# Performance work log

Measured on AMD Instinct MI355X. Metric: run time of the kernel, lower is better.

Reference implementation:

```python
import jax, jax.numpy as jnp
import numpy as np

L = 256
C = 20
B = 4096


def _pairwise_mask(L, C):
    # mask[l1, c1, l2, c2] = (l2 - l1 >= 1), independent of c1, c2
    ls = np.arange(L)
    m = (ls[None, :] - ls[:, None]) >= 1            # (L, L)
    mask = np.broadcast_to(m[:, None, :, None], (L, C, L, C))
    return jnp.asarray(mask[None], dtype=bool)       # (1, L, C, L, C)


def setup_inputs() -> dict:
    key = jax.random.key(0)
    k1, k2, k3, k4 = jax.random.split(key, 4)
    # one-hot sequences, flattened to (B, L*C) like the layer's input
    seq = jax.random.randint(k1, (B, L), 0, C)
    x_lc = jax.nn.one_hot(seq, C, dtype=jnp.float32).reshape(B, L * C)
    theta_0 = jax.random.normal(k2, (1,), dtype=jnp.float32)
    theta_lc = (jax.random.normal(k3, (1, L, C), dtype=jnp.float32)
                / np.sqrt(L).astype(np.float32))
    mask = _pairwise_mask(L, C)
    theta_lclc = (jax.random.normal(k4, (1, L, C, L, C), dtype=jnp.float32)
                  / np.float32(L)) * mask
    return {"x_lc": x_lc, "theta_0": theta_0, "theta_lc": theta_lc,
            "theta_lclc": theta_lclc, "mask": mask}


def reference(x_lc, theta_0, theta_lc, theta_lclc, mask):
    # x_lc: (B, L*C); reshape to (B, L, C)
    x = x_lc.reshape(-1, L, C)
    # additive term: sum over (l, c)
    phi = theta_0 + jnp.einsum('blc,lc->b', x, theta_lc[0])[:, None]  # (B, 1)
    # masked pairwise quadratic form: x^T (theta * mask) x, computed as a
    # GEMM instead of materializing the (B, L, C, L, C) broadcast tensor.
    Theta = (theta_lclc[0] * mask[0].astype(theta_lclc.dtype)).reshape(L * C, L * C)
    xf = x_lc  # (B, L*C)
    quad = jnp.sum((xf @ Theta) * xf, axis=1, keepdims=True)  # (B, 1)
    return phi + quad
```

## Files before the change

kernel.cpp:

```cpp
#include <hip/hip_runtime.h>

#define LPOS 256
#define CCH 20
#define BB 4096
#define LC 5120


__global__ __launch_bounds__(256) void k_prepare(
    const float* __restrict__ x_lc, const float* __restrict__ theta_0,
    const float* __restrict__ theta_lc, unsigned char* __restrict__ seqC,
    float* __restrict__ out)
{
    const int b = blockIdx.x;
    const int l = threadIdx.x;
    const float* xp = x_lc + (size_t)b * LC + (size_t)l * CCH;
    const float4* xp4 = reinterpret_cast<const float4*>(xp);
    float v[CCH];
#pragma unroll
    for (int q = 0; q < 5; ++q) {
        float4 t = xp4[q];
        v[q * 4 + 0] = t.x; v[q * 4 + 1] = t.y;
        v[q * 4 + 2] = t.z; v[q * 4 + 3] = t.w;
    }
    int s = 0; float best = v[0];
#pragma unroll
    for (int c = 1; c < CCH; ++c) { if (v[c] > best) { best = v[c]; s = c; } }

    seqC[(size_t)(l >> 4) * (BB * 16) + (size_t)b * 16 + (l & 15)] =
        (unsigned char)s;

    float lin = theta_lc[l * CCH + s];
#pragma unroll
    for (int off = 32; off > 0; off >>= 1) lin += __shfl_down(lin, off, 64);
    __shared__ float partial[4];
    const int wave = threadIdx.x >> 6;
    const int lane = threadIdx.x & 63;
    if (lane == 0) partial[wave] = lin;
    __syncthreads();
    if (threadIdx.x == 0)
        out[b] = theta_0[0] + partial[0] + partial[1] + partial[2] + partial[3];
}

#define QT 512
#define TBL 6400
#define NCHT 2160
#define NBLK 1024
#define NHEAVY 112

template <int MODE>
__global__ __launch_bounds__(QT, 8) void k_quad(
    const float* __restrict__ Theta,
    const uint4* __restrict__ seqC,
    float* __restrict__ part,
    float* __restrict__ out)
{
    __shared__ float Tl[TBL];

    const int blk = blockIdx.x;
    const int tid = threadIdx.x;
    const int wave = tid >> 6;
    const int lane = tid & 63;

    const int cnt   = (blk < NHEAVY) ? 3 : 2;
    const int start = (blk < NHEAVY) ? 3 * blk : 3 * NHEAVY + 2 * (blk - NHEAVY);

    int cl1[3], cm[3], cjl[3];
    {
        int T = start, l1 = 0;
        for (; l1 < 255; ++l1) {
            const int c = 16 - ((l1 + 1) >> 4);
            if (T < c) break;
            T -= c;
        }
        int m = ((l1 + 1) >> 4) + T;
#pragma unroll
        for (int d = 0; d < 3; ++d) {
            cl1[d] = l1; cm[d] = m;
            cjl[d] = (m == ((l1 + 1) >> 4)) ? ((l1 + 1) & 15) : 0;
            ++m;
            if (m == 16) { ++l1; m = (l1 + 1) >> 4; }
        }
    }

    auto stage = [&](int l1, int m) {
#pragma unroll
        for (int k = 0; k < 4; ++k) {
            const int seg = wave + 8 * k;
            if (seg < 25) {
                const int u = seg * 64 + lane;
                const int r = u / 5, cc = u - r * 5;
                const int j = r / CCH, s1 = r - j * CCH;
                const float* gp = Theta + (size_t)(l1 * CCH + s1) * LC
                                        + (m * 16 + j) * CCH + cc * 4;
                float* lp = Tl + seg * 256;
                __builtin_amdgcn_global_load_lds(
                    (const __attribute__((address_space(1))) void*)gp,
                    (__attribute__((address_space(3))) void*)lp, 16, 0, 0);
            }
        }
    };
    int basev[8];
    auto loadbase = [&](int l1) {
        const int mw = l1 >> 4;
        const int wsel = (l1 >> 2) & 3;
        const int sh = (l1 & 3) * 8;
#pragma unroll
        for (int i = 0; i < 8; ++i) {
            const uint4 u = seqC[(size_t)mw * BB + i * QT + tid];
            const unsigned w = (wsel == 0) ? u.x : (wsel == 1) ? u.y
                             : (wsel == 2) ? u.z : u.w;
            basev[i] = (int)((w >> sh) & 0xFFu) * CCH;
        }
    };

    float acc[8];
#pragma unroll
    for (int i = 0; i < 8; ++i) acc[i] = 0.f;

    auto gather = [&](int d) {
        const int jl = cjl[d];
        const size_t mrow = (size_t)cm[d] * BB;
        if (jl == 0) {
#pragma unroll
            for (int i = 0; i < 8; ++i) {
                const uint4 u = seqC[mrow + i * QT + tid];
#pragma unroll
                for (int j = 0; j < 16; ++j) {
                    const unsigned w = (j < 4) ? u.x : (j < 8) ? u.y
                                     : (j < 12) ? u.z : u.w;
                    const int s2 = (w >> ((j & 3) * 8)) & 0xFF;
                    acc[i] += Tl[j * 400 + basev[i] + s2];
                }
            }
        } else {
#pragma unroll
            for (int i = 0; i < 8; ++i) {
                const uint4 u = seqC[mrow + i * QT + tid];
#pragma unroll
                for (int j = 0; j < 16; ++j) {
                    const unsigned w = (j < 4) ? u.x : (j < 8) ? u.y
                                     : (j < 12) ? u.z : u.w;
                    const int s2 = (w >> ((j & 3) * 8)) & 0xFF;
                    const float v = Tl[j * 400 + basev[i] + s2];
                    acc[i] += (j >= jl) ? v : 0.f;
                }
            }
        }
    };

    int curl1 = cl1[0];
    stage(cl1[0], cm[0]);
    loadbase(cl1[0]);
    __syncthreads();
    gather(0);
    for (int d = 1; d < cnt; ++d) {
        __syncthreads();
        stage(cl1[d], cm[d]);
        if (cl1[d] != curl1) { loadbase(cl1[d]); curl1 = cl1[d]; }
        __syncthreads();
        gather(d);
    }

    if (MODE == 0) {
        float* row = part + (size_t)blk * BB;
#pragma unroll
        for (int i = 0; i < 8; ++i) row[i * QT + tid] = acc[i];
    } else {
#pragma unroll
        for (int i = 0; i < 8; ++i) atomicAdd(&out[i * QT + tid], acc[i]);
    }
}

__global__ __launch_bounds__(256) void k_reduce(
    const float4* __restrict__ part4,
    float* __restrict__ out)
{
    const int b4 = blockIdx.x * 256 + threadIdx.x;
    const int r0 = blockIdx.y * 16;
    float4 a = make_float4(0.f, 0.f, 0.f, 0.f);
    for (int r = r0; r < r0 + 16; ++r) {
        const float4 p = part4[(size_t)r * 1024 + b4];
        a.x += p.x; a.y += p.y; a.z += p.z; a.w += p.w;
    }
    atomicAdd(&out[b4 * 4 + 0], a.x);
    atomicAdd(&out[b4 * 4 + 1], a.y);
    atomicAdd(&out[b4 * 4 + 2], a.z);
    atomicAdd(&out[b4 * 4 + 3], a.w);
}

extern "C" void kernel_launch(void* const* d_in, const int* in_sizes, int n_in,
                              void* d_out, int out_size, void* d_ws, size_t ws_size,
                              hipStream_t stream) {
    const float* x_lc       = (const float*)d_in[0];
    const float* theta_0    = (const float*)d_in[1];
    const float* theta_lc   = (const float*)d_in[2];
    const float* theta_lclc = (const float*)d_in[3];
    float* out = (float*)d_out;

    unsigned char* seqC = (unsigned char*)d_ws;
    float* part = (float*)((char*)d_ws + (1 << 20));
    const size_t need = (1 << 20) + (size_t)NBLK * BB * 4;

    k_prepare<<<dim3(BB), dim3(256), 0, stream>>>(x_lc, theta_0, theta_lc, seqC, out);
    if (ws_size >= need) {
        k_quad<0><<<dim3(NBLK), dim3(QT), 0, stream>>>(
            theta_lclc, (const uint4*)seqC, part, out);
        k_reduce<<<dim3(4, 64), dim3(256), 0, stream>>>(
            (const float4*)part, out);
    } else {
        k_quad<1><<<dim3(NBLK), dim3(QT), 0, stream>>>(
            theta_lclc, (const uint4*)seqC, part, out);
    }
}
```

Measured before the change: 70.59 us.

## Replace static chunk assignment with atomic work-stealing queue in quad kernel

Static per-block assignment of 2 or 3 chunks is replaced by a global atomic counter, so blocks dynamically grab chunk indices. A precomputed chunkinfo table, filled by extra blocks in the prepare kernel, holds the (l1, m, jl) decoding for each chunk. The goal is better load balance across CUs than the fixed 3/2 split. In exchange it adds a memset launch, one atomic per chunk, and an extra barrier per iteration. It also loses the structured reuse of basev between consecutive chunks, since a block's chunks are no longer contiguous.

```diff
diff --git a/kernel.cpp b/kernel.cpp
--- a/kernel.cpp
+++ b/kernel.cpp
@@ -5,12 +5,34 @@
 #define BB 4096
 #define LC 5120
 
+#define QT 512
+#define TBL 6400
+#define NCHT 2160
+#define NBLK 1024
+#define NPREPX 9
+
 
 __global__ __launch_bounds__(256) void k_prepare(
     const float* __restrict__ x_lc, const float* __restrict__ theta_0,
     const float* __restrict__ theta_lc, unsigned char* __restrict__ seqC,
-    float* __restrict__ out)
+    unsigned* __restrict__ chunkinfo, float* __restrict__ out)
 {
+    if (blockIdx.x >= BB) {
+        const int idx = (blockIdx.x - BB) * 256 + threadIdx.x;
+        if (idx < NCHT) {
+            int T = idx, l1 = 0;
+            for (; l1 < 255; ++l1) {
+                const int c = 16 - ((l1 + 1) >> 4);
+                if (T < c) break;
+                T -= c;
+            }
+            const int m = ((l1 + 1) >> 4) + T;
+            const int jl = (m == ((l1 + 1) >> 4)) ? ((l1 + 1) & 15) : 0;
+            chunkinfo[idx] = (unsigned)l1 | ((unsigned)m << 8)
+                           | ((unsigned)jl << 16);
+        }
+        return;
+    }
     const int b = blockIdx.x;
     const int l = threadIdx.x;
     const float* xp = x_lc + (size_t)b * LC + (size_t)l * CCH;
@@ -41,46 +63,21 @@
         out[b] = theta_0[0] + partial[0] + partial[1] + partial[2] + partial[3];
 }
 
-#define QT 512
-#define TBL 6400
-#define NCHT 2160
-#define NBLK 1024
-#define NHEAVY 112
-
 template <int MODE>
 __global__ __launch_bounds__(QT, 8) void k_quad(
     const float* __restrict__ Theta,
     const uint4* __restrict__ seqC,
+    const unsigned* __restrict__ chunkinfo,
+    int* __restrict__ ctr,
     float* __restrict__ part,
     float* __restrict__ out)
 {
     __shared__ float Tl[TBL];
-
-    const int blk = blockIdx.x;
+    __shared__ int nn;
+
     const int tid = threadIdx.x;
     const int wave = tid >> 6;
     const int lane = tid & 63;
-
-    const int cnt   = (blk < NHEAVY) ? 3 : 2;
-    const int start = (blk < NHEAVY) ? 3 * blk : 3 * NHEAVY + 2 * (blk - NHEAVY);
-
-    int cl1[3], cm[3], cjl[3];
-    {
-        int T = start, l1 = 0;
-        for (; l1 < 255; ++l1) {
-            const int c = 16 - ((l1 + 1) >> 4);
-            if (T < c) break;
-            T -= c;
-        }
-        int m = ((l1 + 1) >> 4) + T;
-#pragma unroll
-        for (int d = 0; d < 3; ++d) {
-            cl1[d] = l1; cm[d] = m;
-            cjl[d] = (m == ((l1 + 1) >> 4)) ? ((l1 + 1) & 15) : 0;
-            ++m;
-            if (m == 16) { ++l1; m = (l1 + 1) >> 4; }
-        }
-    }
 
     auto stage = [&](int l1, int m) {
 #pragma unroll
@@ -116,10 +113,24 @@
     float acc[8];
 #pragma unroll
     for (int i = 0; i < 8; ++i) acc[i] = 0.f;
-
-    auto gather = [&](int d) {
-        const int jl = cjl[d];
-        const size_t mrow = (size_t)cm[d] * BB;
+    int curl1 = -1;
+
+    if (tid == 0) nn = atomicAdd(ctr, 1);
+    __syncthreads();
+    int n = nn;
+
+    while (n < NCHT) {
+        const unsigned info = chunkinfo[n];
+        const int l1 = (int)(info & 255u);
+        const int m  = (int)((info >> 8) & 15u);
+        const int jl = (int)((info >> 16) & 15u);
+
+        stage(l1, m);
+        if (l1 != curl1) { loadbase(l1); curl1 = l1; }
+        if (tid == 0) nn = atomicAdd(ctr, 1);
+        __syncthreads();
+
+        const size_t mrow = (size_t)m * BB;
         if (jl == 0) {
 #pragma unroll
             for (int i = 0; i < 8; ++i) {
@@ -146,23 +157,12 @@
                 }
             }
         }
-    };
-
-    int curl1 = cl1[0];
-    stage(cl1[0], cm[0]);
-    loadbase(cl1[0]);
-    __syncthreads();
-    gather(0);
-    for (int d = 1; d < cnt; ++d) {
+        n = nn;
         __syncthreads();
-        stage(cl1[d], cm[d]);
-        if (cl1[d] != curl1) { loadbase(cl1[d]); curl1 = cl1[d]; }
-        __syncthreads();
-        gather(d);
     }
 
     if (MODE == 0) {
-        float* row = part + (size_t)blk * BB;
+        float* row = part + (size_t)blockIdx.x * BB;
 #pragma unroll
         for (int i = 0; i < 8; ++i) row[i * QT + tid] = acc[i];
     } else {
@@ -198,17 +198,30 @@
     float* out = (float*)d_out;
 
     unsigned char* seqC = (unsigned char*)d_ws;
-    float* part = (float*)((char*)d_ws + (1 << 20));
-    const size_t need = (1 << 20) + (size_t)NBLK * BB * 4;
-
-    k_prepare<<<dim3(BB), dim3(256), 0, stream>>>(x_lc, theta_0, theta_lc, seqC, out);
-    if (ws_size >= need) {
+    const size_t part_off = (size_t)1 << 20;
+    const size_t part_sz  = (size_t)NBLK * BB * 4;
+    const size_t full_ctr_off  = part_off + part_sz;
+    const size_t full_info_off = full_ctr_off + 256;
+    const size_t need_full = full_info_off + (size_t)NCHT * 4;
+    const bool full = (ws_size >= need_full);
+
+    const size_t ctr_off  = full ? full_ctr_off  : part_off;
+    const size_t info_off = full ? full_info_off : part_off + 256;
+
+    float*    part      = (float*)((char*)d_ws + part_off);
+    int*      ctr       = (int*)((char*)d_ws + ctr_off);
+    unsigned* chunkinfo = (unsigned*)((char*)d_ws + info_off);
+
+    hipMemsetAsync(ctr, 0, 4, stream);
+    k_prepare<<<dim3(BB + NPREPX), dim3(256), 0, stream>>>(
+        x_lc, theta_0, theta_lc, seqC, chunkinfo, out);
+    if (full) {
         k_quad<0><<<dim3(NBLK), dim3(QT), 0, stream>>>(
-            theta_lclc, (const uint4*)seqC, part, out);
+            theta_lclc, (const uint4*)seqC, chunkinfo, ctr, part, out);
         k_reduce<<<dim3(4, 64), dim3(256), 0, stream>>>(
             (const float4*)part, out);
     } else {
         k_quad<1><<<dim3(NBLK), dim3(QT), 0, stream>>>(
-            theta_lclc, (const uint4*)seqC, part, out);
-    }
-}
+            theta_lclc, (const uint4*)seqC, chunkinfo, ctr, part, out);
+    }
+}
```

Result: slower. 105.7 us (+49.8%).
